# Kernel tuning notes

Hardware: AMD Instinct MI355X
Metric: run time of the kernel (lower is better)

The kernel has to match this reference:

```python
import jax, jax.numpy as jnp
import numpy as np


def setup_inputs() -> dict:
    key = jax.random.key(0)
    k1, k2, k3, k4 = jax.random.split(key, 4)
    n_smps, n_fcns, d_in, d_out = 16384, 2048, 32, 32
    GAIN = 1e-5  # xavier gain used by init_wts / init_offsets
    x = jax.random.normal(k1, (n_smps, d_in), dtype=jnp.float32)
    ctrs = jax.random.normal(k2, (n_fcns, d_in), dtype=jnp.float32)
    wts = jax.random.normal(k3, (n_fcns, d_in, d_out), dtype=jnp.float32) * GAIN
    offsets = jax.random.normal(k4, (n_fcns, d_out), dtype=jnp.float32) * GAIN
    return {"x": x, "ctrs": ctrs, "wts": wts, "offsets": offsets, "k": 4}


def reference(x, ctrs, wts, offsets, k):
    # --- knn_do equivalent (done under no_grad in torch) ---
    # squared Euclidean distance: (n_smps, n_fcns)
    x_sg = jax.lax.stop_gradient(x)
    c_sg = jax.lax.stop_gradient(ctrs)
    d2 = (jnp.sum(x_sg * x_sg, axis=1, keepdims=True)
          - 2.0 * (x_sg @ c_sg.T)
          + jnp.sum(c_sg * c_sg, axis=1)[None, :])
    _, idx = jax.lax.top_k(-d2, k)  # (n_smps, k), nearest centers

    # --- gather per-neighbor local linear models ---
    sel_wts = wts[idx]        # (n_smps, k, d_in, d_out)
    sel_ctrs = ctrs[idx]      # (n_smps, k, d_in)
    sel_offs = offsets[idx]   # (n_smps, k, d_out)

    applied_wts = jnp.sum(sel_wts, axis=1)  # (n_smps, d_in, d_out)
    # offsets minus sum over neighbors/d_in of wts * ctrs
    applied_offsets = (jnp.sum(sel_offs, axis=1)
                       - jnp.einsum('nkde,nkd->ne', sel_wts, sel_ctrs))
    # y = x @ applied_wts + applied_offsets, per sample
    y = jnp.einsum('nde,nd->ne', applied_wts, x) + applied_offsets
    return y
```

## Files before the change

kernel.cpp:

```cpp
#include <hip/hip_runtime.h>
#include <math.h>

typedef short bf16x8 __attribute__((ext_vector_type(8)));
typedef float f32x4  __attribute__((ext_vector_type(4)));
typedef unsigned short ushort_t;

#define N_SMPS 16384
#define N_FCNS 2048
#define D_IN 32
#define D_OUT 32
#define KNN 4
#define SPLITS 4
#define CPS 512
#define TILES 32

__device__ __forceinline__ unsigned umin_u(unsigned a, unsigned b) { return a < b ? a : b; }
__device__ __forceinline__ unsigned umax_u(unsigned a, unsigned b) { return a > b ? a : b; }

__device__ __forceinline__ ushort_t bf16_rne(float f) {
  unsigned b = __float_as_uint(f);
  unsigned r = b + 0x7FFFu + ((b >> 16) & 1u);
  return (ushort_t)(r >> 16);
}

#define OFF_XH   0u
#define OFF_XL   (1u << 20)
#define OFF_CH   (2u << 20)
#define OFF_CL   (OFF_CH + 131072u)
#define OFF_HB   (OFF_CL + 131072u)
#define OFF_CAND (OFF_HB + 8192u)
#define OFF_IDX  (OFF_CAND + (SPLITS * N_SMPS * 32u))

__global__ __launch_bounds__(256) void k_prep(
    const float* __restrict__ x, const float* __restrict__ ctrs,
    ushort_t* __restrict__ xh, ushort_t* __restrict__ xl,
    ushort_t* __restrict__ ch, ushort_t* __restrict__ cl,
    float* __restrict__ hb)
{
  const int gt = blockIdx.x * 256 + threadIdx.x;
  const int NX4 = N_SMPS * D_IN / 4;
  const int NC4 = N_FCNS * D_IN / 4;

  const float* src; ushort_t* dh; ushort_t* dl; int i4;
  if (gt < NX4) { src = x; dh = xh; dl = xl; i4 = gt; }
  else          { src = ctrs; dh = ch; dl = cl; i4 = gt - NX4; }
  if (gt < NX4 + NC4) {
    float4 v = ((const float4*)src)[i4];
    float vv[4] = {v.x, v.y, v.z, v.w};
    ushort_t h[4], l[4];
    #pragma unroll
    for (int q = 0; q < 4; ++q) {
      ushort_t hh = bf16_rne(vv[q]);
      float hf = __uint_as_float(((unsigned)hh) << 16);
      h[q] = hh;
      l[q] = bf16_rne(vv[q] - hf);
    }
    ushort_t* ph = dh + 4 * i4; ushort_t* pl = dl + 4 * i4;
    #pragma unroll
    for (int q = 0; q < 4; ++q) { ph[q] = h[q]; pl[q] = l[q]; }
  }
  if (gt < N_FCNS) {
    const float4* cp4 = (const float4*)(ctrs + (size_t)gt * D_IN);
    float a = 0.f;
    #pragma unroll
    for (int q = 0; q < 8; ++q) {
      float4 v = cp4[q];
      a += v.x * v.x + v.y * v.y + v.z * v.z + v.w * v.w;
    }
    hb[gt] = -0.5f * a;
  }
}

__global__ __launch_bounds__(256, 4) void k_topk(
    const ushort_t* __restrict__ xh, const ushort_t* __restrict__ xl,
    const ushort_t* __restrict__ ch, const ushort_t* __restrict__ cl,
    const float* __restrict__ hb, unsigned* __restrict__ cand)
{
  __shared__ unsigned s_mrg[4][16 * 68];

  const int tid = threadIdx.x;
  const int lane = tid & 63;
  const int w = __builtin_amdgcn_readfirstlane(tid >> 6);
  const int col = lane & 15;
  const int quad = lane >> 4;
  const int sbase = blockIdx.x * 16;
  const int nbase0 = w * CPS;

  const bf16x8 ah = *(const bf16x8*)(xh + (size_t)(sbase + col) * D_IN + quad * 8);
  const bf16x8 al = *(const bf16x8*)(xl + (size_t)(sbase + col) * D_IN + quad * 8);

  unsigned ls[4][4];
  #pragma unroll
  for (int r = 0; r < 4; ++r)
    #pragma unroll
    for (int e = 0; e < 4; ++e) ls[r][e] = 0u;

  #pragma unroll 2
  for (int t = 0; t < TILES; ++t) {
    const int nb = nbase0 + t * 16;
    const bf16x8 bh = *(const bf16x8*)(ch + (size_t)(nb + col) * D_IN + quad * 8);
    const bf16x8 bl = *(const bf16x8*)(cl + (size_t)(nb + col) * D_IN + quad * 8);
    const float hbv = hb[nb + col];
    f32x4 acc = {0.f, 0.f, 0.f, 0.f};
    acc = __builtin_amdgcn_mfma_f32_16x16x32_bf16(ah, bh, acc, 0, 0, 0);
    acc = __builtin_amdgcn_mfma_f32_16x16x32_bf16(ah, bl, acc, 0, 0, 0);
    acc = __builtin_amdgcn_mfma_f32_16x16x32_bf16(al, bh, acc, 0, 0, 0);
    acc = __builtin_amdgcn_mfma_f32_16x16x32_bf16(al, bl, acc, 0, 0, 0);
    const unsigned tc = (unsigned)(t * 16 + col);
    #pragma unroll
    for (int r = 0; r < 4; ++r) {
      const float u = acc[r] + hbv;
      unsigned b = __float_as_uint(u);
      unsigned m = b ^ ((unsigned)((int)b >> 31) | 0x80000000u);
      unsigned key = (m & 0xFFFFFE00u) | tc;
      unsigned t0 = umin_u(ls[r][0], key); ls[r][0] = umax_u(ls[r][0], key);
      unsigned t1 = umin_u(ls[r][1], t0);  ls[r][1] = umax_u(ls[r][1], t0);
      unsigned t2 = umin_u(ls[r][2], t1);  ls[r][2] = umax_u(ls[r][2], t1);
      ls[r][3] = umax_u(ls[r][3], t2);
    }
  }

  unsigned* mrg = s_mrg[w];
  #pragma unroll
  for (int r = 0; r < 4; ++r) {
    const int row = quad * 4 + r;
    *(uint4*)(mrg + row * 68 + col * 4) =
        make_uint4(ls[r][0], ls[r][1], ls[r][2], ls[r][3]);
  }
  __syncthreads();

  if (lane < 16) {
    unsigned q0 = 0, q1 = 0, q2 = 0, q3 = 0, q4 = 0, q5 = 0;
    const uint4* rp = (const uint4*)(mrg + lane * 68);
    #pragma unroll
    for (int c2 = 0; c2 < 16; ++c2) {
      uint4 kv = rp[c2];
      unsigned ks[4] = {kv.x, kv.y, kv.z, kv.w};
      #pragma unroll
      for (int e = 0; e < 4; ++e) {
        unsigned key = ks[e];
        unsigned t0 = umin_u(q0, key); q0 = umax_u(q0, key);
        unsigned t1 = umin_u(q1, t0);  q1 = umax_u(q1, t0);
        unsigned t2 = umin_u(q2, t1);  q2 = umax_u(q2, t1);
        unsigned t3 = umin_u(q3, t2);  q3 = umax_u(q3, t2);
        unsigned t4 = umin_u(q4, t3);  q4 = umax_u(q4, t3);
        q5 = umax_u(q5, t4);
      }
    }
    unsigned* op = cand + ((size_t)w * N_SMPS + sbase + lane) * 8;
    *(uint4*)op = make_uint4(q0, q1, q2, q3);
    *(uint2*)(op + 4) = make_uint2(q4, q5);
  }
}

#define KM_BLOCK 128

__global__ __launch_bounds__(KM_BLOCK) void k_merge(
    const float* __restrict__ x, const float* __restrict__ ctrs,
    const unsigned* __restrict__ cand, int* __restrict__ idx_out)
{
  const int s = blockIdx.x * KM_BLOCK + threadIdx.x;

  int nn[SPLITS * 6];
  #pragma unroll
  for (int sp = 0; sp < SPLITS; ++sp) {
    const unsigned* ip = cand + ((size_t)sp * N_SMPS + s) * 8;
    uint4 a = *(const uint4*)ip;
    uint2 b = *(const uint2*)(ip + 4);
    nn[sp * 6 + 0] = sp * CPS + (int)(a.x & 0x1FFu);
    nn[sp * 6 + 1] = sp * CPS + (int)(a.y & 0x1FFu);
    nn[sp * 6 + 2] = sp * CPS + (int)(a.z & 0x1FFu);
    nn[sp * 6 + 3] = sp * CPS + (int)(a.w & 0x1FFu);
    nn[sp * 6 + 4] = sp * CPS + (int)(b.x & 0x1FFu);
    nn[sp * 6 + 5] = sp * CPS + (int)(b.y & 0x1FFu);
  }

  double xd[D_IN];
  {
    const float4* xp = (const float4*)(x + (size_t)s * D_IN);
    #pragma unroll
    for (int q = 0; q < 8; ++q) {
      float4 v = xp[q];
      xd[4 * q + 0] = (double)v.x; xd[4 * q + 1] = (double)v.y;
      xd[4 * q + 2] = (double)v.z; xd[4 * q + 3] = (double)v.w;
    }
  }

  double bd[4]; int b4[4];
  #pragma unroll
  for (int e = 0; e < 4; ++e) { bd[e] = 1e300; b4[e] = 0x7fffffff; }
  for (int m = 0; m < SPLITS * 6; ++m) {
    const int j = nn[m];
    const float* cp = ctrs + (size_t)j * D_IN;
    double d2a = 0.0, d2b = 0.0;
    #pragma unroll
    for (int d = 0; d < D_IN; d += 2) {
      double df0 = xd[d] - (double)cp[d];
      double df1 = xd[d + 1] - (double)cp[d + 1];
      d2a = fma(df0, df0, d2a);
      d2b = fma(df1, df1, d2b);
    }
    double d2 = d2a + d2b;
    bool ins = (d2 < bd[3]) || (d2 == bd[3] && j < b4[3]);
    if (ins) {
      bd[3] = d2; b4[3] = j;
      #pragma unroll
      for (int q = 3; q > 0; --q) {
        bool sw = (bd[q] < bd[q - 1]) || (bd[q] == bd[q - 1] && b4[q] < b4[q - 1]);
        if (sw) {
          double td = bd[q]; bd[q] = bd[q - 1]; bd[q - 1] = td;
          int    tj = b4[q]; b4[q] = b4[q - 1]; b4[q - 1] = tj;
        }
      }
    }
  }
  #pragma unroll
  for (int q = 0; q < 4; ++q) idx_out[s * KNN + q] = b4[q];
}

#define K2_BLOCK 256
#define K2_SAMPLES 8

__global__ __launch_bounds__(K2_BLOCK) void k_apply(
    const float* __restrict__ x, const float* __restrict__ ctrs,
    const float* __restrict__ wts, const float* __restrict__ offs,
    const int* __restrict__ idx, float* __restrict__ y)
{
  __shared__ float  s_diff[K2_SAMPLES][KNN][D_IN + 1];
  __shared__ float4 s_part[K2_SAMPLES][KNN][D_OUT / 4];
  const int tid = threadIdx.x;
  const int sbase = blockIdx.x * K2_SAMPLES;

  #pragma unroll
  for (int r = 0; r < K2_SAMPLES * KNN * D_IN / K2_BLOCK; ++r) {
    int v = r * K2_BLOCK + tid;
    int d = v & 31; int p = v >> 5;
    int sl = p >> 2; int j = p & 3;
    int f = idx[(sbase + sl) * KNN + j];
    s_diff[sl][j][d] =
        x[(size_t)(sbase + sl) * D_IN + d] - ctrs[(size_t)f * D_IN + d];
  }
  __syncthreads();

  const int sl = tid >> 5;
  const int j  = (tid >> 3) & 3;
  const int eq = tid & 7;
  const int s = sbase + sl;

  const int f = idx[s * KNN + j];
  const float4* wp = (const float4*)(wts + (size_t)f * (D_IN * D_OUT));
  float4 acc = ((const float4*)(offs + (size_t)f * D_OUT))[eq];
  #pragma unroll
  for (int d = 0; d < D_IN; ++d) {
    float4 wv = wp[d * (D_OUT / 4) + eq];
    float xc = s_diff[sl][j][d];
    acc.x = fmaf(xc, wv.x, acc.x);
    acc.y = fmaf(xc, wv.y, acc.y);
    acc.z = fmaf(xc, wv.z, acc.z);
    acc.w = fmaf(xc, wv.w, acc.w);
  }
  s_part[sl][j][eq] = acc;
  __syncthreads();

  if (j == 0) {
    float4 a = s_part[sl][0][eq], b = s_part[sl][1][eq];
    float4 c = s_part[sl][2][eq], e = s_part[sl][3][eq];
    float4 o;
    o.x = (a.x + b.x) + (c.x + e.x);
    o.y = (a.y + b.y) + (c.y + e.y);
    o.z = (a.z + b.z) + (c.z + e.z);
    o.w = (a.w + b.w) + (c.w + e.w);
    ((float4*)(y + (size_t)s * D_OUT))[eq] = o;
  }
}

extern "C" void kernel_launch(void* const* d_in, const int* in_sizes, int n_in,
                              void* d_out, int out_size, void* d_ws, size_t ws_size,
                              hipStream_t stream) {
  const float* x    = (const float*)d_in[0];
  const float* ctrs = (const float*)d_in[1];
  const float* wts  = (const float*)d_in[2];
  const float* offs = (const float*)d_in[3];
  float* y = (float*)d_out;

  char* ws = (char*)d_ws;
  ushort_t* xh = (ushort_t*)(ws + OFF_XH);
  ushort_t* xl = (ushort_t*)(ws + OFF_XL);
  ushort_t* ch = (ushort_t*)(ws + OFF_CH);
  ushort_t* cl = (ushort_t*)(ws + OFF_CL);
  float*    hb = (float*)(ws + OFF_HB);
  unsigned* cand = (unsigned*)(ws + OFF_CAND);
  int*    idxb = (int*)(ws + OFF_IDX);

  k_prep<<<(N_SMPS * D_IN / 4 + N_FCNS * D_IN / 4) / 256, 256, 0, stream>>>(
      x, ctrs, xh, xl, ch, cl, hb);
  k_topk<<<N_SMPS / 16, 256, 0, stream>>>(xh, xl, ch, cl, hb, cand);
  k_merge<<<N_SMPS / KM_BLOCK, KM_BLOCK, 0, stream>>>(x, ctrs, cand, idxb);
  k_apply<<<N_SMPS / K2_SAMPLES, K2_BLOCK, 0, stream>>>(x, ctrs, wts, offs,
                                                        idxb, y);
}
```

Before: 135.4 us.

## Invert apply stage to per-center grouping with counting sort and reduction

Replaces the per-sample apply kernel, which gathered each neighbor's 4KB weight matrix from global memory, with an inverted scheme. Neighbor pairs are counted per center, prefix-scanned and bucketed, and then one block per center loads its weights into shared memory once and applies them to all assigned samples. Partial outputs go to a workspace buffer and a final kernel sums the four neighbors. This removes redundant weight traffic but adds atomics, extra launches including a single-block scan, and load imbalance across centers.

```diff
diff --git a/kernel.cpp b/kernel.cpp
--- a/kernel.cpp
+++ b/kernel.cpp
@@ -13,6 +13,7 @@
 #define SPLITS 4
 #define CPS 512
 #define TILES 32
+#define NPAIR (N_SMPS * KNN)
 
 __device__ __forceinline__ unsigned umin_u(unsigned a, unsigned b) { return a < b ? a : b; }
 __device__ __forceinline__ unsigned umax_u(unsigned a, unsigned b) { return a > b ? a : b; }
@@ -30,6 +31,11 @@
 #define OFF_HB   (OFF_CL + 131072u)
 #define OFF_CAND (OFF_HB + 8192u)
 #define OFF_IDX  (OFF_CAND + (SPLITS * N_SMPS * 32u))
+#define OFF_CNT  (OFF_IDX + (NPAIR * 4u))
+#define OFF_CNT2 (OFF_CNT + 8192u)
+#define OFF_BASE (OFF_CNT2 + 8192u)
+#define OFF_LIST (OFF_BASE + 8448u)
+#define OFF_PART (OFF_LIST + (NPAIR * 4u))
 
 __global__ __launch_bounds__(256) void k_prep(
     const float* __restrict__ x, const float* __restrict__ ctrs,
@@ -157,7 +163,8 @@
 
 __global__ __launch_bounds__(KM_BLOCK) void k_merge(
     const float* __restrict__ x, const float* __restrict__ ctrs,
-    const unsigned* __restrict__ cand, int* __restrict__ idx_out)
+    const unsigned* __restrict__ cand, int* __restrict__ idx_out,
+    int* __restrict__ cnt)
 {
   const int s = blockIdx.x * KM_BLOCK + threadIdx.x;
 
@@ -215,63 +222,107 @@
     }
   }
   #pragma unroll
-  for (int q = 0; q < 4; ++q) idx_out[s * KNN + q] = b4[q];
-}
-
-#define K2_BLOCK 256
-#define K2_SAMPLES 8
-
-__global__ __launch_bounds__(K2_BLOCK) void k_apply(
+  for (int q = 0; q < 4; ++q) {
+    idx_out[s * KNN + q] = b4[q];
+    atomicAdd(&cnt[b4[q]], 1);
+  }
+}
+
+__global__ __launch_bounds__(256) void k_scan(
+    const int* __restrict__ cnt, int* __restrict__ base)
+{
+  __shared__ int s_sum[256];
+  const int tid = threadIdx.x;
+  int loc[8]; int acc = 0;
+  #pragma unroll
+  for (int q = 0; q < 8; ++q) { loc[q] = acc; acc += cnt[tid * 8 + q]; }
+  s_sum[tid] = acc;
+  __syncthreads();
+  #pragma unroll
+  for (int off = 1; off < 256; off <<= 1) {
+    int v = (tid >= off) ? s_sum[tid - off] : 0;
+    __syncthreads();
+    s_sum[tid] += v;
+    __syncthreads();
+  }
+  const int pre = (tid == 0) ? 0 : s_sum[tid - 1];
+  #pragma unroll
+  for (int q = 0; q < 8; ++q) base[tid * 8 + q] = pre + loc[q];
+  if (tid == 255) base[N_FCNS] = pre + acc;
+}
+
+__global__ __launch_bounds__(256) void k_place(
+    const int* __restrict__ idx, const int* __restrict__ base,
+    int* __restrict__ cnt2, int* __restrict__ list)
+{
+  const int t = blockIdx.x * 256 + threadIdx.x;
+  const int f = idx[t];
+  const int pos = base[f] + atomicAdd(&cnt2[f], 1);
+  list[pos] = t;
+}
+
+__global__ __launch_bounds__(256) void k_apply_inv(
     const float* __restrict__ x, const float* __restrict__ ctrs,
     const float* __restrict__ wts, const float* __restrict__ offs,
-    const int* __restrict__ idx, float* __restrict__ y)
-{
-  __shared__ float  s_diff[K2_SAMPLES][KNN][D_IN + 1];
-  __shared__ float4 s_part[K2_SAMPLES][KNN][D_OUT / 4];
+    const int* __restrict__ base, const int* __restrict__ list,
+    float* __restrict__ part)
+{
+  __shared__ float s_w[D_IN * D_OUT];
+  __shared__ float s_diff[8][D_IN + 1];
+
+  const int f = blockIdx.x;
   const int tid = threadIdx.x;
-  const int sbase = blockIdx.x * K2_SAMPLES;
-
-  #pragma unroll
-  for (int r = 0; r < K2_SAMPLES * KNN * D_IN / K2_BLOCK; ++r) {
-    int v = r * K2_BLOCK + tid;
-    int d = v & 31; int p = v >> 5;
-    int sl = p >> 2; int j = p & 3;
-    int f = idx[(sbase + sl) * KNN + j];
-    s_diff[sl][j][d] =
-        x[(size_t)(sbase + sl) * D_IN + d] - ctrs[(size_t)f * D_IN + d];
-  }
+  const int si = tid >> 5;
+  const int c = tid & 31;
+
+  {
+    const float4* wg = (const float4*)(wts + (size_t)f * (D_IN * D_OUT));
+    ((float4*)s_w)[tid] = wg[tid];
+  }
+  const float creg = ctrs[(size_t)f * D_IN + c];
+  const float offc = offs[(size_t)f * D_OUT + c];
+  const int start = base[f];
+  const int n = base[f + 1] - start;
   __syncthreads();
 
-  const int sl = tid >> 5;
-  const int j  = (tid >> 3) & 3;
-  const int eq = tid & 7;
-  const int s = sbase + sl;
-
-  const int f = idx[s * KNN + j];
-  const float4* wp = (const float4*)(wts + (size_t)f * (D_IN * D_OUT));
-  float4 acc = ((const float4*)(offs + (size_t)f * D_OUT))[eq];
-  #pragma unroll
-  for (int d = 0; d < D_IN; ++d) {
-    float4 wv = wp[d * (D_OUT / 4) + eq];
-    float xc = s_diff[sl][j][d];
-    acc.x = fmaf(xc, wv.x, acc.x);
-    acc.y = fmaf(xc, wv.y, acc.y);
-    acc.z = fmaf(xc, wv.z, acc.z);
-    acc.w = fmaf(xc, wv.w, acc.w);
-  }
-  s_part[sl][j][eq] = acc;
-  __syncthreads();
-
-  if (j == 0) {
-    float4 a = s_part[sl][0][eq], b = s_part[sl][1][eq];
-    float4 c = s_part[sl][2][eq], e = s_part[sl][3][eq];
-    float4 o;
-    o.x = (a.x + b.x) + (c.x + e.x);
-    o.y = (a.y + b.y) + (c.y + e.y);
-    o.z = (a.z + b.z) + (c.z + e.z);
-    o.w = (a.w + b.w) + (c.w + e.w);
-    ((float4*)(y + (size_t)s * D_OUT))[eq] = o;
-  }
+  for (int i0 = 0; i0 < n; i0 += 8) {
+    const int i = i0 + si;
+    int sv = -1;
+    if (i < n) sv = list[start + i];
+    if (sv >= 0) {
+      const int s = sv >> 2;
+      s_diff[si][c] = x[(size_t)s * D_IN + c] - creg;
+    }
+    __syncthreads();
+    if (sv >= 0) {
+      float a0 = offc, a1 = 0.f, a2 = 0.f, a3 = 0.f;
+      #pragma unroll
+      for (int d = 0; d < D_IN; d += 4) {
+        a0 = fmaf(s_diff[si][d + 0], s_w[(d + 0) * D_OUT + c], a0);
+        a1 = fmaf(s_diff[si][d + 1], s_w[(d + 1) * D_OUT + c], a1);
+        a2 = fmaf(s_diff[si][d + 2], s_w[(d + 2) * D_OUT + c], a2);
+        a3 = fmaf(s_diff[si][d + 3], s_w[(d + 3) * D_OUT + c], a3);
+      }
+      part[(size_t)sv * D_OUT + c] = (a0 + a1) + (a2 + a3);
+    }
+    __syncthreads();
+  }
+}
+
+__global__ __launch_bounds__(256) void k_reduce(
+    const float* __restrict__ part, float* __restrict__ y)
+{
+  const int t = blockIdx.x * 256 + threadIdx.x;
+  const int s = t >> 3;
+  const int c4 = t & 7;
+  const float4* p = (const float4*)(part + (size_t)s * 4 * D_OUT) + c4;
+  float4 a = p[0], b = p[8], c = p[16], e = p[24];
+  float4 o;
+  o.x = (a.x + b.x) + (c.x + e.x);
+  o.y = (a.y + b.y) + (c.y + e.y);
+  o.z = (a.z + b.z) + (c.z + e.z);
+  o.w = (a.w + b.w) + (c.w + e.w);
+  ((float4*)(y + (size_t)s * D_OUT))[c4] = o;
 }
 
 extern "C" void kernel_launch(void* const* d_in, const int* in_sizes, int n_in,
@@ -291,11 +342,19 @@
   float*    hb = (float*)(ws + OFF_HB);
   unsigned* cand = (unsigned*)(ws + OFF_CAND);
   int*    idxb = (int*)(ws + OFF_IDX);
-
+  int*    cnt  = (int*)(ws + OFF_CNT);
+  int*    cnt2 = (int*)(ws + OFF_CNT2);
+  int*    base = (int*)(ws + OFF_BASE);
+  int*    list = (int*)(ws + OFF_LIST);
+  float*  part = (float*)(ws + OFF_PART);
+
+  hipMemsetAsync(cnt, 0, 16384, stream);
   k_prep<<<(N_SMPS * D_IN / 4 + N_FCNS * D_IN / 4) / 256, 256, 0, stream>>>(
       x, ctrs, xh, xl, ch, cl, hb);
   k_topk<<<N_SMPS / 16, 256, 0, stream>>>(xh, xl, ch, cl, hb, cand);
-  k_merge<<<N_SMPS / KM_BLOCK, KM_BLOCK, 0, stream>>>(x, ctrs, cand, idxb);
-  k_apply<<<N_SMPS / K2_SAMPLES, K2_BLOCK, 0, stream>>>(x, ctrs, wts, offs,
-                                                        idxb, y);
-}
+  k_merge<<<N_SMPS / KM_BLOCK, KM_BLOCK, 0, stream>>>(x, ctrs, cand, idxb, cnt);
+  k_scan<<<1, 256, 0, stream>>>(cnt, base);
+  k_place<<<NPAIR / 256, 256, 0, stream>>>(idxb, base, cnt2, list);
+  k_apply_inv<<<N_FCNS, 256, 0, stream>>>(x, ctrs, wts, offs, base, list, part);
+  k_reduce<<<(N_SMPS * 8) / 256, 256, 0, stream>>>(part, y);
+}
```

Measured after the change: 220.7 us. 1.63x slower.

## Fuse prep, top-k and merge into one kNN kernel with single bf16 MFMA

Applied to the files above, without the earlier changes.

Removes the separate bf16 split/prep kernel and the global candidate buffer by converting x and centers to bf16 inside the top-k kernel and computing center norms on the fly with lane shuffles. Drops the three error-compensation MFMAs, relying on a larger candidate pool (6 per 8-lane group, 48 per sample) to be rescored exactly in double precision. The final merge now runs within the same block via shared memory. This cuts launches and global traffic, but adds per-tile conversion and norm work, and makes candidate selection less precise, so a true neighbour could in principle be missed.

```diff
diff --git a/kernel.cpp b/kernel.cpp
--- a/kernel.cpp
+++ b/kernel.cpp
@@ -3,7 +3,6 @@
 
 typedef short bf16x8 __attribute__((ext_vector_type(8)));
 typedef float f32x4  __attribute__((ext_vector_type(4)));
-typedef unsigned short ushort_t;
 
 #define N_SMPS 16384
 #define N_FCNS 2048
@@ -13,70 +12,24 @@
 #define SPLITS 4
 #define CPS 512
 #define TILES 32
+#define POOL 48
 
 __device__ __forceinline__ unsigned umin_u(unsigned a, unsigned b) { return a < b ? a : b; }
 __device__ __forceinline__ unsigned umax_u(unsigned a, unsigned b) { return a > b ? a : b; }
 
-__device__ __forceinline__ ushort_t bf16_rne(float f) {
+__device__ __forceinline__ unsigned short bf16_rne(float f) {
   unsigned b = __float_as_uint(f);
   unsigned r = b + 0x7FFFu + ((b >> 16) & 1u);
-  return (ushort_t)(r >> 16);
-}
-
-#define OFF_XH   0u
-#define OFF_XL   (1u << 20)
-#define OFF_CH   (2u << 20)
-#define OFF_CL   (OFF_CH + 131072u)
-#define OFF_HB   (OFF_CL + 131072u)
-#define OFF_CAND (OFF_HB + 8192u)
-#define OFF_IDX  (OFF_CAND + (SPLITS * N_SMPS * 32u))
-
-__global__ __launch_bounds__(256) void k_prep(
+  return (unsigned short)(r >> 16);
+}
+
+__global__ __launch_bounds__(256, 4) void k_knn(
     const float* __restrict__ x, const float* __restrict__ ctrs,
-    ushort_t* __restrict__ xh, ushort_t* __restrict__ xl,
-    ushort_t* __restrict__ ch, ushort_t* __restrict__ cl,
-    float* __restrict__ hb)
+    int* __restrict__ idx_out)
 {
-  const int gt = blockIdx.x * 256 + threadIdx.x;
-  const int NX4 = N_SMPS * D_IN / 4;
-  const int NC4 = N_FCNS * D_IN / 4;
-
-  const float* src; ushort_t* dh; ushort_t* dl; int i4;
-  if (gt < NX4) { src = x; dh = xh; dl = xl; i4 = gt; }
-  else          { src = ctrs; dh = ch; dl = cl; i4 = gt - NX4; }
-  if (gt < NX4 + NC4) {
-    float4 v = ((const float4*)src)[i4];
-    float vv[4] = {v.x, v.y, v.z, v.w};
-    ushort_t h[4], l[4];
-    #pragma unroll
-    for (int q = 0; q < 4; ++q) {
-      ushort_t hh = bf16_rne(vv[q]);
-      float hf = __uint_as_float(((unsigned)hh) << 16);
-      h[q] = hh;
-      l[q] = bf16_rne(vv[q] - hf);
-    }
-    ushort_t* ph = dh + 4 * i4; ushort_t* pl = dl + 4 * i4;
-    #pragma unroll
-    for (int q = 0; q < 4; ++q) { ph[q] = h[q]; pl[q] = l[q]; }
-  }
-  if (gt < N_FCNS) {
-    const float4* cp4 = (const float4*)(ctrs + (size_t)gt * D_IN);
-    float a = 0.f;
-    #pragma unroll
-    for (int q = 0; q < 8; ++q) {
-      float4 v = cp4[q];
-      a += v.x * v.x + v.y * v.y + v.z * v.z + v.w * v.w;
-    }
-    hb[gt] = -0.5f * a;
-  }
-}
-
-__global__ __launch_bounds__(256, 4) void k_topk(
-    const ushort_t* __restrict__ xh, const ushort_t* __restrict__ xl,
-    const ushort_t* __restrict__ ch, const ushort_t* __restrict__ cl,
-    const float* __restrict__ hb, unsigned* __restrict__ cand)
-{
-  __shared__ unsigned s_mrg[4][16 * 68];
+  __shared__ unsigned s_cand[SPLITS][16][16][4];
+  __shared__ double   s_d2[16][POOL];
+  __shared__ int      s_ix[16][POOL];
 
   const int tid = threadIdx.x;
   const int lane = tid & 63;
@@ -86,8 +39,15 @@
   const int sbase = blockIdx.x * 16;
   const int nbase0 = w * CPS;
 
-  const bf16x8 ah = *(const bf16x8*)(xh + (size_t)(sbase + col) * D_IN + quad * 8);
-  const bf16x8 al = *(const bf16x8*)(xl + (size_t)(sbase + col) * D_IN + quad * 8);
+  bf16x8 ah;
+  {
+    const float4* xp =
+        (const float4*)(x + (size_t)(sbase + col) * D_IN + quad * 8);
+    float4 v0 = xp[0], v1 = xp[1];
+    float xf[8] = {v0.x, v0.y, v0.z, v0.w, v1.x, v1.y, v1.z, v1.w};
+    #pragma unroll
+    for (int i = 0; i < 8; ++i) ah[i] = (short)bf16_rne(xf[i]);
+  }
 
   unsigned ls[4][4];
   #pragma unroll
@@ -97,15 +57,23 @@
 
   #pragma unroll 2
   for (int t = 0; t < TILES; ++t) {
-    const int nb = nbase0 + t * 16;
-    const bf16x8 bh = *(const bf16x8*)(ch + (size_t)(nb + col) * D_IN + quad * 8);
-    const bf16x8 bl = *(const bf16x8*)(cl + (size_t)(nb + col) * D_IN + quad * 8);
-    const float hbv = hb[nb + col];
+    const int row = nbase0 + t * 16 + col;
+    const float4* cp = (const float4*)(ctrs + (size_t)row * D_IN + quad * 8);
+    float4 c0 = cp[0], c1 = cp[1];
+    float cf[8] = {c0.x, c0.y, c0.z, c0.w, c1.x, c1.y, c1.z, c1.w};
+    bf16x8 bh;
+    #pragma unroll
+    for (int i = 0; i < 8; ++i) bh[i] = (short)bf16_rne(cf[i]);
+    float pn = 0.f;
+    #pragma unroll
+    for (int i = 0; i < 8; ++i) pn = fmaf(cf[i], cf[i], pn);
+    pn += __shfl_xor(pn, 16, 64);
+    pn += __shfl_xor(pn, 32, 64);
+    const float hbv = -0.5f * pn;
+
     f32x4 acc = {0.f, 0.f, 0.f, 0.f};
     acc = __builtin_amdgcn_mfma_f32_16x16x32_bf16(ah, bh, acc, 0, 0, 0);
-    acc = __builtin_amdgcn_mfma_f32_16x16x32_bf16(ah, bl, acc, 0, 0, 0);
-    acc = __builtin_amdgcn_mfma_f32_16x16x32_bf16(al, bh, acc, 0, 0, 0);
-    acc = __builtin_amdgcn_mfma_f32_16x16x32_bf16(al, bl, acc, 0, 0, 0);
+
     const unsigned tc = (unsigned)(t * 16 + col);
     #pragma unroll
     for (int r = 0; r < 4; ++r) {
@@ -120,21 +88,23 @@
     }
   }
 
-  unsigned* mrg = s_mrg[w];
   #pragma unroll
   for (int r = 0; r < 4; ++r) {
     const int row = quad * 4 + r;
-    *(uint4*)(mrg + row * 68 + col * 4) =
+    *(uint4*)&s_cand[w][row][col][0] =
         make_uint4(ls[r][0], ls[r][1], ls[r][2], ls[r][3]);
   }
   __syncthreads();
 
-  if (lane < 16) {
+  if (tid < 128) {
+    const int sl = tid >> 3;
+    const int g  = tid & 7;
+    const int wv = g >> 1;
+    const int ch = (g & 1) * 8;
     unsigned q0 = 0, q1 = 0, q2 = 0, q3 = 0, q4 = 0, q5 = 0;
-    const uint4* rp = (const uint4*)(mrg + lane * 68);
-    #pragma unroll
-    for (int c2 = 0; c2 < 16; ++c2) {
-      uint4 kv = rp[c2];
+    #pragma unroll
+    for (int c2 = 0; c2 < 8; ++c2) {
+      uint4 kv = *(const uint4*)&s_cand[wv][sl][ch + c2][0];
       unsigned ks[4] = {kv.x, kv.y, kv.z, kv.w};
       #pragma unroll
       for (int e = 0; e < 4; ++e) {
@@ -147,75 +117,56 @@
         q5 = umax_u(q5, t4);
       }
     }
-    unsigned* op = cand + ((size_t)w * N_SMPS + sbase + lane) * 8;
-    *(uint4*)op = make_uint4(q0, q1, q2, q3);
-    *(uint2*)(op + 4) = make_uint2(q4, q5);
-  }
-}
-
-#define KM_BLOCK 128
-
-__global__ __launch_bounds__(KM_BLOCK) void k_merge(
-    const float* __restrict__ x, const float* __restrict__ ctrs,
-    const unsigned* __restrict__ cand, int* __restrict__ idx_out)
-{
-  const int s = blockIdx.x * KM_BLOCK + threadIdx.x;
-
-  int nn[SPLITS * 6];
-  #pragma unroll
-  for (int sp = 0; sp < SPLITS; ++sp) {
-    const unsigned* ip = cand + ((size_t)sp * N_SMPS + s) * 8;
-    uint4 a = *(const uint4*)ip;
-    uint2 b = *(const uint2*)(ip + 4);
-    nn[sp * 6 + 0] = sp * CPS + (int)(a.x & 0x1FFu);
-    nn[sp * 6 + 1] = sp * CPS + (int)(a.y & 0x1FFu);
-    nn[sp * 6 + 2] = sp * CPS + (int)(a.z & 0x1FFu);
-    nn[sp * 6 + 3] = sp * CPS + (int)(a.w & 0x1FFu);
-    nn[sp * 6 + 4] = sp * CPS + (int)(b.x & 0x1FFu);
-    nn[sp * 6 + 5] = sp * CPS + (int)(b.y & 0x1FFu);
-  }
-
-  double xd[D_IN];
-  {
-    const float4* xp = (const float4*)(x + (size_t)s * D_IN);
-    #pragma unroll
-    for (int q = 0; q < 8; ++q) {
-      float4 v = xp[q];
-      xd[4 * q + 0] = (double)v.x; xd[4 * q + 1] = (double)v.y;
-      xd[4 * q + 2] = (double)v.z; xd[4 * q + 3] = (double)v.w;
-    }
-  }
-
-  double bd[4]; int b4[4];
-  #pragma unroll
-  for (int e = 0; e < 4; ++e) { bd[e] = 1e300; b4[e] = 0x7fffffff; }
-  for (int m = 0; m < SPLITS * 6; ++m) {
-    const int j = nn[m];
-    const float* cp = ctrs + (size_t)j * D_IN;
-    double d2a = 0.0, d2b = 0.0;
-    #pragma unroll
-    for (int d = 0; d < D_IN; d += 2) {
-      double df0 = xd[d] - (double)cp[d];
-      double df1 = xd[d + 1] - (double)cp[d + 1];
-      d2a = fma(df0, df0, d2a);
-      d2b = fma(df1, df1, d2b);
-    }
-    double d2 = d2a + d2b;
-    bool ins = (d2 < bd[3]) || (d2 == bd[3] && j < b4[3]);
-    if (ins) {
-      bd[3] = d2; b4[3] = j;
+    unsigned sel[6] = {q0, q1, q2, q3, q4, q5};
+    const float4* xp4 = (const float4*)(x + (size_t)(sbase + sl) * D_IN);
+    #pragma unroll
+    for (int i = 0; i < 6; ++i) {
+      const int j = wv * CPS + (int)(sel[i] & 0x1FFu);
+      const float4* cp4 = (const float4*)(ctrs + (size_t)j * D_IN);
+      double d2a = 0.0, d2b = 0.0;
       #pragma unroll
-      for (int q = 3; q > 0; --q) {
-        bool sw = (bd[q] < bd[q - 1]) || (bd[q] == bd[q - 1] && b4[q] < b4[q - 1]);
-        if (sw) {
-          double td = bd[q]; bd[q] = bd[q - 1]; bd[q - 1] = td;
-          int    tj = b4[q]; b4[q] = b4[q - 1]; b4[q - 1] = tj;
+      for (int q = 0; q < 8; ++q) {
+        float4 cv = cp4[q];
+        float4 xv = xp4[q];
+        double df0 = (double)xv.x - (double)cv.x;
+        double df1 = (double)xv.y - (double)cv.y;
+        double df2 = (double)xv.z - (double)cv.z;
+        double df3 = (double)xv.w - (double)cv.w;
+        d2a = fma(df0, df0, d2a);
+        d2b = fma(df1, df1, d2b);
+        d2a = fma(df2, df2, d2a);
+        d2b = fma(df3, df3, d2b);
+      }
+      s_d2[sl][g * 6 + i] = d2a + d2b;
+      s_ix[sl][g * 6 + i] = j;
+    }
+  }
+  __syncthreads();
+
+  if (tid < 16) {
+    double bd[4]; int b4[4];
+    #pragma unroll
+    for (int e = 0; e < 4; ++e) { bd[e] = 1e300; b4[e] = 0x7fffffff; }
+    for (int m = 0; m < POOL; ++m) {
+      const double d2 = s_d2[tid][m];
+      const int j = s_ix[tid][m];
+      bool ins = (d2 < bd[3]) || (d2 == bd[3] && j < b4[3]);
+      if (ins) {
+        bd[3] = d2; b4[3] = j;
+        #pragma unroll
+        for (int q = 3; q > 0; --q) {
+          bool sw = (bd[q] < bd[q - 1]) ||
+                    (bd[q] == bd[q - 1] && b4[q] < b4[q - 1]);
+          if (sw) {
+            double td = bd[q]; bd[q] = bd[q - 1]; bd[q - 1] = td;
+            int    tj = b4[q]; b4[q] = b4[q - 1]; b4[q - 1] = tj;
+          }
         }
       }
     }
-  }
-  #pragma unroll
-  for (int q = 0; q < 4; ++q) idx_out[s * KNN + q] = b4[q];
+    #pragma unroll
+    for (int q = 0; q < 4; ++q) idx_out[(sbase + tid) * KNN + q] = b4[q];
+  }
 }
 
 #define K2_BLOCK 256
@@ -282,20 +233,9 @@
   const float* wts  = (const float*)d_in[2];
   const float* offs = (const float*)d_in[3];
   float* y = (float*)d_out;
-
-  char* ws = (char*)d_ws;
-  ushort_t* xh = (ushort_t*)(ws + OFF_XH);
-  ushort_t* xl = (ushort_t*)(ws + OFF_XL);
-  ushort_t* ch = (ushort_t*)(ws + OFF_CH);
-  ushort_t* cl = (ushort_t*)(ws + OFF_CL);
-  float*    hb = (float*)(ws + OFF_HB);
-  unsigned* cand = (unsigned*)(ws + OFF_CAND);
-  int*    idxb = (int*)(ws + OFF_IDX);
-
-  k_prep<<<(N_SMPS * D_IN / 4 + N_FCNS * D_IN / 4) / 256, 256, 0, stream>>>(
-      x, ctrs, xh, xl, ch, cl, hb);
-  k_topk<<<N_SMPS / 16, 256, 0, stream>>>(xh, xl, ch, cl, hb, cand);
-  k_merge<<<N_SMPS / KM_BLOCK, KM_BLOCK, 0, stream>>>(x, ctrs, cand, idxb);
+  int* idxb = (int*)d_ws;
+
+  k_knn<<<N_SMPS / 16, 256, 0, stream>>>(x, ctrs, idxb);
   k_apply<<<N_SMPS / K2_SAMPLES, K2_BLOCK, 0, stream>>>(x, ctrs, wts, offs,
                                                         idxb, y);
 }
```

Result: slower. 161.1 us (+18.9%).
